# Kernel tuning notes

Measured on AMD Instinct MI355X. Metric: run time of the kernel, lower is better.

Reference implementation:

```python
import jax, jax.numpy as jnp
import numpy as np
import math

B, NRES, RPR = 1, 384, 3
L = NRES * RPR          # 1152 rigids
CS, CZ = 256, 128
CH, H, PQ, PV = 16, 8, 8, 12


def _ln(x, scale, bias):
    mu = jnp.mean(x, axis=-1, keepdims=True)
    var = jnp.var(x, axis=-1, keepdims=True)
    return (x - mu) * jax.lax.rsqrt(var + 1e-5) * scale + bias


def _quat_to_rot(q):
    q = q / jnp.linalg.norm(q, axis=-1, keepdims=True)
    w, x, y, z = q[..., 0], q[..., 1], q[..., 2], q[..., 3]
    r = jnp.stack([
        1 - 2 * (y * y + z * z), 2 * (x * y - w * z), 2 * (x * z + w * y),
        2 * (x * y + w * z), 1 - 2 * (x * x + z * z), 2 * (y * z - w * x),
        2 * (x * z - w * y), 2 * (y * z + w * x), 1 - 2 * (x * x + y * y),
    ], axis=-1)
    return r.reshape(q.shape[:-1] + (3, 3))


def setup_inputs() -> dict:
    key = jax.random.key(0)
    ks = jax.random.split(key, 20)
    s = jax.random.normal(ks[0], (B, L, CS), jnp.float32)
    z = jax.random.normal(ks[1], (B, NRES, NRES, CZ), jnp.float32)
    rot = _quat_to_rot(jax.random.normal(ks[2], (B, L, 4), jnp.float32))
    trans = 10.0 * jax.random.normal(ks[3], (B, L, 3), jnp.float32)
    mask = jnp.ones((B, L), jnp.float32)
    rigid_to_res_idx = jnp.broadcast_to(jnp.arange(L, dtype=jnp.int32) // RPR, (B, L))
    w = lambda k, sh: 0.02 * jax.random.normal(k, sh, jnp.float32)
    return {
        "s": s, "z": z, "rot": rot, "trans": trans, "mask": mask,
        "ln_s_scale": jnp.ones((CS,), jnp.float32), "ln_s_bias": jnp.zeros((CS,), jnp.float32),
        "ln_z_scale": jnp.ones((CZ,), jnp.float32), "ln_z_bias": jnp.zeros((CZ,), jnp.float32),
        "w_q": w(ks[4], (CS, H * CH)), "w_k": w(ks[5], (CS, H * CH)), "w_v": w(ks[6], (CS, H * CH)),
        "w_qp": w(ks[7], (CS, H * PQ * 3)), "w_kp": w(ks[8], (CS, H * PQ * 3)), "w_vp": w(ks[9], (CS, H * PV * 3)),
        "w_b": w(ks[10], (CZ, H)),
        "head_weights": jnp.full((H,), 0.5413, jnp.float32),  # softplus^-1(1)
        "w_out": w(ks[11], (H * (CH + CZ + PV * 4), CS)),
        "b_out": jnp.zeros((CS,), jnp.float32),
        "rigid_to_res_idx": rigid_to_res_idx,
    }


def reference(s, z, rot, trans, mask, ln_s_scale, ln_s_bias, ln_z_scale, ln_z_bias,
              w_q, w_k, w_v, w_qp, w_kp, w_vp, w_b, head_weights, w_out, b_out,
              rigid_to_res_idx):
    b_, l_ = s.shape[0], s.shape[1]
    idx = rigid_to_res_idx[0]                       # [L] rigid -> residue, shared over batch
    s_ln = _ln(s, ln_s_scale, ln_s_bias)            # [B,L,CS]
    z_ln = _ln(z, ln_z_scale, ln_z_bias)            # [B,N,N,CZ]

    q = (s_ln @ w_q).reshape(b_, l_, H, CH)
    k = (s_ln @ w_k).reshape(b_, l_, H, CH)
    v = (s_ln @ w_v).reshape(b_, l_, H, CH)

    # local points, then rigid-transform to global frame: x_g = R x + t
    q_p = (s_ln @ w_qp).reshape(b_, l_, H, PQ, 3)
    k_p = (s_ln @ w_kp).reshape(b_, l_, H, PQ, 3)
    v_p = (s_ln @ w_vp).reshape(b_, l_, H, PV, 3)
    t5 = trans[:, :, None, None, :]
    q_g = jnp.einsum("blij,blhpj->blhpi", rot, q_p) + t5
    k_g = jnp.einsum("blij,blhpj->blhpi", rot, k_p) + t5
    v_g = jnp.einsum("blij,blhpj->blhpi", rot, v_p) + t5

    # scalar qk term
    a = jnp.einsum("blhc,bjhc->bhlj", q, k) * math.sqrt(1.0 / (3 * CH))
    # pair bias, broadcast residue-pair -> rigid-pair
    b_res = z_ln @ w_b                                # [B,N,N,H]
    b_full = b_res[:, idx][:, :, idx]                 # [B,L,L,H]
    a = a + math.sqrt(1.0 / 3) * jnp.transpose(b_full, (0, 3, 1, 2))
    # point-distance term: ||q-k||^2 = |q|^2 + |k|^2 - 2 q.k (summed over P,3)
    hw = jax.nn.softplus(head_weights) * math.sqrt(1.0 / (3 * (PQ * 9.0 / 2)))
    qq = jnp.sum(q_g * q_g, axis=(-1, -2)).transpose(0, 2, 1)   # [B,H,L]
    kk = jnp.sum(k_g * k_g, axis=(-1, -2)).transpose(0, 2, 1)
    qk = jnp.einsum("blhpc,bjhpc->bhlj", q_g, k_g)
    d2 = qq[:, :, :, None] + kk[:, :, None, :] - 2.0 * qk
    a = a - 0.5 * d2 * hw[None, :, None, None]
    a = a + (mask[:, None, None, :] - 1.0) * 1e9
    attn = jax.nn.softmax(a, axis=-1)                 # [B,H,L,L]

    o = jnp.einsum("bhlj,bjhc->blhc", attn, v)        # [B,L,H,CH]
    o_pt_g = jnp.einsum("bhlj,bjhpc->blhpc", attn, v_g)
    # back to local frame of query rigid: R^T (x - t)
    o_pt = jnp.einsum("blji,blhpj->blhpi", rot, o_pt_g - t5)
    o_pt_norm = jnp.sqrt(jnp.sum(o_pt * o_pt, axis=-1) + 1e-8)  # [B,L,H,PV]
    # pair output: sum attention over rigids belonging to each key residue
    attn_res = attn.reshape(b_, H, l_, NRES, RPR).sum(-1)       # [B,H,L,N]
    z_l = z_ln[:, idx]                                           # [B,L,N,CZ]
    o_pair = jnp.einsum("bhln,blnc->blhc", attn_res, z_l)        # [B,L,H,CZ]

    cat = jnp.concatenate(
        [o, o_pt.reshape(b_, l_, H, PV * 3), o_pt_norm, o_pair], axis=-1
    ).reshape(b_, l_, H * (CH + PV * 4 + CZ))
    return cat @ w_out + b_out                        # [B,L,CS]
```

## Files before the change

kernel.cpp:

```cpp
#include <hip/hip_runtime.h>
#include <hip/hip_bf16.h>

#define L 1152
#define NRES 384
#define CS 256
#define CZ 128
#define H 8
#define CH 16
#define PQ 8
#define PV 12
#define PSTR 1088

#define OFF_SLN  0L
#define OFF_PROJ 294912L
#define OFF_WPK  1548288L
#define OFF_QCAT 1826816L
#define OFF_KCAT 2232320L
#define OFF_VCAT 2637824L
#define OFF_BRES 3227648L
#define OFF_MURS 4407296L
#define OFF_ATTN 4702208L
#define OFF_CAT  15319040L
#define OFF_PAV  18286592L
#define OFF_POP  21825536L
#define OFF_ARES 26544128L
#define OFF_PCAT 30083072L
#define OFF_RST  32442368L

__global__ __launch_bounds__(256) void k_pre(
    const float* wq, const float* wk, const float* wv,
    const float* wqp, const float* wkp, const float* wvp, float* wpack,
    const float* s, const float* lnss, const float* lnsb, float* sln,
    const float* z, const float* lnzs, const float* lnzb,
    const float* wb, float* murs, float* bres_t){
  int bx = blockIdx.x, t = threadIdx.x;
  if(bx < 256){
    int k = bx;
    for(int c=t; c<PSTR; c+=256){
      float v;
      if(c<128)        v = wq [(long)k*128 + c];
      else if(c<256)   v = wk [(long)k*128 + c-128];
      else if(c<384)   v = wv [(long)k*128 + c-256];
      else if(c<576)   v = wqp[(long)k*192 + c-384];
      else if(c<768)   v = wkp[(long)k*192 + c-576];
      else if(c<1056)  v = wvp[(long)k*288 + c-768];
      else             v = 0.f;
      wpack[(long)k*PSTR + c] = v;
    }
    return;
  }
  if(bx < 256 + L){
    int l = bx - 256;
    __shared__ float red[CS];
    float x = s[(long)l*CS + t];
    red[t] = x; __syncthreads();
    for(int st=128; st>0; st>>=1){ if(t<st) red[t]+=red[t+st]; __syncthreads(); }
    float mu = red[0] * (1.f/CS); __syncthreads();
    float d = x - mu;
    red[t] = d*d; __syncthreads();
    for(int st=128; st>0; st>>=1){ if(t<st) red[t]+=red[t+st]; __syncthreads(); }
    float var = red[0]*(1.f/CS);
    sln[(long)l*CS + t] = d*rsqrtf(var + 1e-5f)*lnss[t] + lnsb[t];
    return;
  }
  {
    long rp0 = (long)(bx - 256 - L)*32;
    int r = t>>3, part = t&7;
    long rp = rp0 + r;
    __shared__ __align__(16) float swb[8*132];
    __shared__ float SB[8][2];
    const float4* z4 = (const float4*)z;
    float4 x0 = z4[rp*32 + part*4 + 0];
    float4 x1 = z4[rp*32 + part*4 + 1];
    float4 x2 = z4[rp*32 + part*4 + 2];
    float4 x3 = z4[rp*32 + part*4 + 3];
    #pragma unroll
    for(int k2=0;k2<4;k2++){
      int e = t + k2*256; int h = e>>7, c = e&127;
      swb[h*132 + c] = lnzs[c]*wb[(long)c*8 + h];
    }
    __syncthreads();
    if(t < 64){
      int h = t>>3, seg = t&7;
      float S=0, Bv=0;
      #pragma unroll
      for(int i=0;i<16;i++){
        int c = seg*16+i;
        S  += swb[h*132+c];
        Bv += lnzb[c]*wb[(long)c*8 + h];
      }
      #pragma unroll
      for(int off=1;off<8;off<<=1){ S += __shfl_xor(S,off,64); Bv += __shfl_xor(Bv,off,64); }
      if(seg==0){ SB[h][0]=S; SB[h][1]=Bv; }
    }
    float s1 = x0.x+x0.y+x0.z+x0.w + x1.x+x1.y+x1.z+x1.w
             + x2.x+x2.y+x2.z+x2.w + x3.x+x3.y+x3.z+x3.w;
    float s2 = x0.x*x0.x+x0.y*x0.y+x0.z*x0.z+x0.w*x0.w
             + x1.x*x1.x+x1.y*x1.y+x1.z*x1.z+x1.w*x1.w
             + x2.x*x2.x+x2.y*x2.y+x2.z*x2.z+x2.w*x2.w
             + x3.x*x3.x+x3.y*x3.y+x3.z*x3.z+x3.w*x3.w;
    #pragma unroll
    for(int off=1;off<8;off<<=1){ s1 += __shfl_xor(s1,off,64); s2 += __shfl_xor(s2,off,64); }
    float mu = s1*(1.f/CZ);
    float var = s2*(1.f/CZ) - mu*mu;
    float rstd = rsqrtf(var + 1e-5f);
    if(part==0){ murs[rp*2]=mu; murs[rp*2+1]=rstd; }
    float acc[8];
    const float4* swb4 = (const float4*)swb;
    #pragma unroll
    for(int h=0;h<8;h++){
      float4 wa = swb4[h*33 + part*4 + 0];
      float4 wbv= swb4[h*33 + part*4 + 1];
      float4 wc = swb4[h*33 + part*4 + 2];
      float4 wd = swb4[h*33 + part*4 + 3];
      acc[h] = x0.x*wa.x + x0.y*wa.y + x0.z*wa.z + x0.w*wa.w
             + x1.x*wbv.x+ x1.y*wbv.y+ x1.z*wbv.z+ x1.w*wbv.w
             + x2.x*wc.x + x2.y*wc.y + x2.z*wc.z + x2.w*wc.w
             + x3.x*wd.x + x3.y*wd.y + x3.z*wd.z + x3.w*wd.w;
    }
    #pragma unroll
    for(int off=1;off<8;off<<=1){
      #pragma unroll
      for(int h=0;h<8;h++) acc[h] += __shfl_xor(acc[h],off,64);
    }
    __syncthreads();
    if(part==0){
      #pragma unroll
      for(int h=0;h<8;h++)
        bres_t[(long)h*147456 + rp] = rstd*(acc[h] - mu*SB[h][0]) + SB[h][1];
    }
  }
}

__global__ __launch_bounds__(256) void k_proj(const float* sln, const float* wpack, float* proj){
  int l0 = blockIdx.x*64, c0 = blockIdx.y*64, t = threadIdx.x;
  __shared__ float a_s[32][68];
  __shared__ __align__(16) float w_s[32][68];
  int tr = t>>4, tc = t&15;
  float4 acc[4] = {{0,0,0,0},{0,0,0,0},{0,0,0,0},{0,0,0,0}};
  for(int kc=0; kc<8; kc++){
    int k0 = kc*32;
    {
      int row = t>>2, kk0 = (t&3)*8;
      const float4* src = (const float4*)(sln + (long)(l0+row)*256 + k0 + kk0);
      float4 v0 = src[0], v1 = src[1];
      a_s[kk0+0][row]=v0.x; a_s[kk0+1][row]=v0.y; a_s[kk0+2][row]=v0.z; a_s[kk0+3][row]=v0.w;
      a_s[kk0+4][row]=v1.x; a_s[kk0+5][row]=v1.y; a_s[kk0+6][row]=v1.z; a_s[kk0+7][row]=v1.w;
    }
    #pragma unroll
    for(int kk2=0; kk2<2; kk2++){
      int kk = (t>>4) + 16*kk2;
      *(float4*)&w_s[kk][(t&15)*4] = *(const float4*)(wpack + (long)(k0+kk)*PSTR + c0 + (t&15)*4);
    }
    __syncthreads();
    #pragma unroll 8
    for(int kk=0; kk<32; kk++){
      float4 a4 = *(const float4*)&a_s[kk][tr*4];
      float4 b4 = *(const float4*)&w_s[kk][tc*4];
      acc[0].x+=a4.x*b4.x; acc[0].y+=a4.x*b4.y; acc[0].z+=a4.x*b4.z; acc[0].w+=a4.x*b4.w;
      acc[1].x+=a4.y*b4.x; acc[1].y+=a4.y*b4.y; acc[1].z+=a4.y*b4.z; acc[1].w+=a4.y*b4.w;
      acc[2].x+=a4.z*b4.x; acc[2].y+=a4.z*b4.y; acc[2].z+=a4.z*b4.z; acc[2].w+=a4.z*b4.w;
      acc[3].x+=a4.w*b4.x; acc[3].y+=a4.w*b4.y; acc[3].z+=a4.w*b4.z; acc[3].w+=a4.w*b4.w;
    }
    __syncthreads();
  }
  #pragma unroll
  for(int r=0;r<4;r++)
    *(float4*)(proj + (long)(l0 + tr*4 + r)*PSTR + c0 + tc*4) = acc[r];
}

__global__ __launch_bounds__(256) void k_rigid(const float* proj, const float* rot, const float* trans,
                        const float* mask, const float* hws,
                        float* qcat, float* kcat, float* vcat){
  int l = blockIdx.x, t = threadIdx.x;
  __shared__ float R[9], T[3], hwS[8], qgs[192], kgs[192];
  if(t<9) R[t]=rot[(long)l*9+t];
  if(t<3) T[t]=trans[(long)l*3+t];
  if(t>=16 && t<24) hwS[t-16] = log1pf(expf(hws[t-16]))*0.09622504486493764f;
  __syncthreads();
  const float* pr = proj + (long)l*PSTR;
  if(t<128){
    int h=t>>4, c=t&15;
    qcat[((long)h*44 + c)*L + l] = 0.14433756729740643f * pr[t];
    kcat[((long)h*44 + c)*L + l] = pr[128+t];
    vcat[((long)h*L + l)*64 + c] = pr[256+t];
  }
  if(t < 192){
    int h=t/24, m=t%24, p=m/3, i=m%3;
    float qa = R[i*3+0]*pr[384+h*24+p*3+0] + R[i*3+1]*pr[384+h*24+p*3+1]
             + R[i*3+2]*pr[384+h*24+p*3+2] + T[i];
    float ka = R[i*3+0]*pr[576+h*24+p*3+0] + R[i*3+1]*pr[576+h*24+p*3+1]
             + R[i*3+2]*pr[576+h*24+p*3+2] + T[i];
    qgs[t]=qa; kgs[t]=ka;
    qcat[((long)h*44 + 16 + m)*L + l] = hwS[h]*qa;
    kcat[((long)h*44 + 16 + m)*L + l] = ka;
  }
  for(int it=t; it<288; it+=256){
    int h=it/36, m=it%36, p=m/3, i=m%3;
    float a = R[i*3+0]*pr[768+h*36+p*3+0] + R[i*3+1]*pr[768+h*36+p*3+1]
            + R[i*3+2]*pr[768+h*36+p*3+2] + T[i];
    vcat[((long)h*L + l)*64 + 16 + m] = a;
  }
  if(t < 96){
    int h=t/12, d=t%12;
    vcat[((long)h*L + l)*64 + 52 + d] = 0.f;
  }
  __syncthreads();
  if(t < 8){
    float qq=0, kk=0;
    #pragma unroll
    for(int m=0;m<24;m++){ qq += qgs[t*24+m]*qgs[t*24+m]; kk += kgs[t*24+m]*kgs[t*24+m]; }
    qcat[((long)t*44 + 40)*L + l] = -0.5f*hwS[t]*qq;
    kcat[((long)t*44 + 40)*L + l] = -0.5f*hwS[t]*kk + (mask[l]-1.f)*1e9f;
  }
}

__global__ __launch_bounds__(256) void k_scores(const float* qcat, const float* kcat,
                         const float* bres_t, float* attn){
  int l0 = blockIdx.x*32, j0 = blockIdx.y*128, h = blockIdx.z;
  int t = threadIdx.x;
  __shared__ __align__(16) float q_t[44*36];
  __shared__ __align__(16) float k_t[44*132];
  __shared__ float bp[12*44];
  int rl0 = l0/3, rj0 = j0/3;
  {
    const float* srcq = qcat + (long)h*44*L + l0;
    for(int i=t; i<44*32; i+=256){
      int c = i>>5, ll = i&31;
      q_t[c*36 + ll] = srcq[(long)c*L + ll];
    }
    const float* srck = kcat + (long)h*44*L + j0;
    for(int i=t; i<44*128; i+=256){
      int c = i>>7, jj = i&127;
      k_t[c*132 + jj] = srck[(long)c*L + jj];
    }
    const float* bb = bres_t + (long)h*147456;
    for(int i=t; i<12*44; i+=256){
      int r = i/44, c = i-r*44;
      int rr = rl0+r, cc = rj0+c;
      bp[i] = (rr<NRES && cc<NRES) ? bb[(long)rr*NRES + cc] : 0.f;
    }
  }
  __syncthreads();
  int lg = t>>5, jg = t&31;
  float acc[4][4] = {};
  #pragma unroll 4
  for(int c=0;c<40;c++){
    float4 qv = *(const float4*)&q_t[c*36 + lg*4];
    float4 kv = *(const float4*)&k_t[c*132 + jg*4];
    acc[0][0]+=qv.x*kv.x; acc[0][1]+=qv.x*kv.y; acc[0][2]+=qv.x*kv.z; acc[0][3]+=qv.x*kv.w;
    acc[1][0]+=qv.y*kv.x; acc[1][1]+=qv.y*kv.y; acc[1][2]+=qv.y*kv.z; acc[1][3]+=qv.y*kv.w;
    acc[2][0]+=qv.z*kv.x; acc[2][1]+=qv.z*kv.y; acc[2][2]+=qv.z*kv.z; acc[2][3]+=qv.z*kv.w;
    acc[3][0]+=qv.w*kv.x; acc[3][1]+=qv.w*kv.y; acc[3][2]+=qv.w*kv.z; acc[3][3]+=qv.w*kv.w;
  }
  float4 colc = *(const float4*)&k_t[40*132 + jg*4];
  int jb = j0 + jg*4;
  int rj0i = (jb  )/3 - rj0;
  int rj1i = (jb+1)/3 - rj0;
  int rj2i = (jb+2)/3 - rj0;
  int rj3i = (jb+3)/3 - rj0;
  #pragma unroll
  for(int r=0;r<4;r++){
    int row = lg*4+r;
    float rowc = q_t[40*36 + row];
    const float* bpr = &bp[((l0+row)/3 - rl0)*44];
    float4 o;
    o.x = __expf(acc[r][0] + rowc + colc.x + 0.5773502691896258f*bpr[rj0i]);
    o.y = __expf(acc[r][1] + rowc + colc.y + 0.5773502691896258f*bpr[rj1i]);
    o.z = __expf(acc[r][2] + rowc + colc.z + 0.5773502691896258f*bpr[rj2i]);
    o.w = __expf(acc[r][3] + rowc + colc.w + 0.5773502691896258f*bpr[rj3i]);
    *(float4*)(attn + ((long)h*L + l0+row)*L + jb) = o;
  }
}

__global__ __launch_bounds__(256) void k_rowstat(const float* attn, float* rstat, float* ares){
  long row = (long)blockIdx.x*4 + (threadIdx.x>>6);
  int lane = threadIdx.x & 63;
  int w = threadIdx.x >> 6;
  __shared__ float es[4][1152];
  const float* p = attn + row*L;
  float v[18];
  float s=0;
  #pragma unroll
  for(int i=0;i<18;i++){ v[i]=p[lane + i*64]; s+=v[i]; }
  #pragma unroll
  for(int off=1;off<64;off<<=1) s+=__shfl_xor(s,off,64);
  float inv = 1.f/s;
  if(lane==0) rstat[row] = inv;
  #pragma unroll
  for(int i=0;i<18;i++) es[w][lane + i*64] = v[i]*inv;
  __syncthreads();
  #pragma unroll
  for(int q=0;q<6;q++){
    int n = lane + q*64;
    ares[row*NRES + n] = es[w][3*n] + es[w][3*n+1] + es[w][3*n+2];
  }
}

__global__ __launch_bounds__(256) void k_av(const float* attn, const float* vcat,
                     const float* rstat, float* pav){
  int lb = blockIdx.x, h = blockIdx.y, sp = blockIdx.z, t = threadIdx.x;
  int l0 = lb*64;
  __shared__ __align__(16) float a_s[64][68];
  __shared__ __align__(16) float v_s[64][68];
  int lgrp = t>>4, dgrp = t&15;
  float4 acc[4] = {{0,0,0,0},{0,0,0,0},{0,0,0,0},{0,0,0,0}};
  const float* abase = attn + ((long)h*L + l0)*L;
  int al = t>>2, jj0s = (t&3)*16;
  float irow = rstat[(long)h*L + l0 + al];
  for(int jc=sp*3; jc<sp*3+3; jc++){
    int j0 = jc*64;
    {
      const float4* src = (const float4*)(abase + (long)al*L + j0 + jj0s);
      float4 p0 = src[0], p1 = src[1], p2 = src[2], p3 = src[3];
      a_s[jj0s+ 0][al]=p0.x*irow; a_s[jj0s+ 1][al]=p0.y*irow;
      a_s[jj0s+ 2][al]=p0.z*irow; a_s[jj0s+ 3][al]=p0.w*irow;
      a_s[jj0s+ 4][al]=p1.x*irow; a_s[jj0s+ 5][al]=p1.y*irow;
      a_s[jj0s+ 6][al]=p1.z*irow; a_s[jj0s+ 7][al]=p1.w*irow;
      a_s[jj0s+ 8][al]=p2.x*irow; a_s[jj0s+ 9][al]=p2.y*irow;
      a_s[jj0s+10][al]=p2.z*irow; a_s[jj0s+11][al]=p2.w*irow;
      a_s[jj0s+12][al]=p3.x*irow; a_s[jj0s+13][al]=p3.y*irow;
      a_s[jj0s+14][al]=p3.z*irow; a_s[jj0s+15][al]=p3.w*irow;
    }
    {
      int jj = t>>2, seg = t&3;
      const float4* src = (const float4*)(vcat + ((long)h*L + j0 + jj)*64 + seg*16);
      float4 q0=src[0], q1=src[1], q2=src[2], q3=src[3];
      float4* dst = (float4*)&v_s[jj][seg*16];
      dst[0]=q0; dst[1]=q1; dst[2]=q2; dst[3]=q3;
    }
    __syncthreads();
    #pragma unroll 8
    for(int jj=0; jj<64; jj++){
      float4 av = *(const float4*)&a_s[jj][lgrp*4];
      float4 vv = *(const float4*)&v_s[jj][dgrp*4];
      acc[0].x+=av.x*vv.x; acc[0].y+=av.x*vv.y; acc[0].z+=av.x*vv.z; acc[0].w+=av.x*vv.w;
      acc[1].x+=av.y*vv.x; acc[1].y+=av.y*vv.y; acc[1].z+=av.y*vv.z; acc[1].w+=av.y*vv.w;
      acc[2].x+=av.z*vv.x; acc[2].y+=av.z*vv.y; acc[2].z+=av.z*vv.z; acc[2].w+=av.z*vv.w;
      acc[3].x+=av.w*vv.x; acc[3].y+=av.w*vv.y; acc[3].z+=av.w*vv.z; acc[3].w+=av.w*vv.w;
    }
    __syncthreads();
  }
  #pragma unroll
  for(int r=0;r<4;r++)
    *(float4*)(pav + (((long)sp*H + h)*L + l0 + lgrp*4 + r)*64 + dgrp*4) = acc[r];
}

#define OPAIR_STEP(Z0,Z1,Z2,Z3,NB) { \
    float4 a0 = *(const float4*)&ar[0][th][NB]; \
    float4 a1 = *(const float4*)&ar[1][th][NB]; \
    float4 a2 = *(const float4*)&ar[2][th][NB]; \
    acc[0][0] += a0.x*Z0.x + a0.y*Z1.x + a0.z*Z2.x + a0.w*Z3.x; \
    acc[0][1] += a0.x*Z0.y + a0.y*Z1.y + a0.z*Z2.y + a0.w*Z3.y; \
    acc[0][2] += a0.x*Z0.z + a0.y*Z1.z + a0.z*Z2.z + a0.w*Z3.z; \
    acc[0][3] += a0.x*Z0.w + a0.y*Z1.w + a0.z*Z2.w + a0.w*Z3.w; \
    acc[1][0] += a1.x*Z0.x + a1.y*Z1.x + a1.z*Z2.x + a1.w*Z3.x; \
    acc[1][1] += a1.x*Z0.y + a1.y*Z1.y + a1.z*Z2.y + a1.w*Z3.y; \
    acc[1][2] += a1.x*Z0.z + a1.y*Z1.z + a1.z*Z2.z + a1.w*Z3.z; \
    acc[1][3] += a1.x*Z0.w + a1.y*Z1.w + a1.z*Z2.w + a1.w*Z3.w; \
    acc[2][0] += a2.x*Z0.x + a2.y*Z1.x + a2.z*Z2.x + a2.w*Z3.x; \
    acc[2][1] += a2.x*Z0.y + a2.y*Z1.y + a2.z*Z2.y + a2.w*Z3.y; \
    acc[2][2] += a2.x*Z0.z + a2.y*Z1.z + a2.z*Z2.z + a2.w*Z3.z; \
    acc[2][3] += a2.x*Z0.w + a2.y*Z1.w + a2.z*Z2.w + a2.w*Z3.w; }

__global__ __launch_bounds__(256) void k_opair(const float* ares, const float* z, const float* murs,
                        const float* sc, const int* ridx, float* po){
  int r=blockIdx.x, sp=blockIdx.y, t=threadIdx.x;
  __shared__ __align__(16) float ar[3][H][96];
  __shared__ __align__(16) float mrs[96*2];
  __shared__ float S1s[24];
  int rl = ridx[r*3];
  int n0 = sp*96;
  int tc = t&31, th = t>>5;
  const float* zbase = z + ((long)(rl*NRES + n0))*CZ + tc*4;
  float4 zc0 = *(const float4*)(zbase + 0L*CZ);
  float4 zc1 = *(const float4*)(zbase + 1L*CZ);
  float4 zc2 = *(const float4*)(zbase + 2L*CZ);
  float4 zc3 = *(const float4*)(zbase + 3L*CZ);
  for(int i=t;i<192;i+=256) mrs[i]=murs[((long)rl*NRES + n0)*2 + i];
  __syncthreads();
  for(int it=t; it<3*H*96; it+=256){
    int lo = it/(H*96);
    int rem = it - lo*(H*96);
    int h = rem/96, n = rem - h*96;
    ar[lo][h][n] = ares[((long)h*L + r*3+lo)*NRES + n0 + n] * mrs[n*2+1];
  }
  __syncthreads();
  if(t<192){
    int row=t>>3, seg=t&7;
    const float* arr = ((const float*)ar) + row*96 + seg*12;
    const float* mur = mrs + seg*24;
    float s1=0;
    #pragma unroll
    for(int q2=0;q2<12;q2++) s1 += arr[q2]*mur[q2*2];
    s1 += __shfl_xor(s1,1,64); s1 += __shfl_xor(s1,2,64); s1 += __shfl_xor(s1,4,64);
    if(seg==0) S1s[row]=s1;
  }
  __syncthreads();
  float acc[3][4]={};
  for(int nb=0; nb<88; nb+=8){
    float4 zn0 = *(const float4*)(zbase + (long)(nb+4)*CZ);
    float4 zn1 = *(const float4*)(zbase + (long)(nb+5)*CZ);
    float4 zn2 = *(const float4*)(zbase + (long)(nb+6)*CZ);
    float4 zn3 = *(const float4*)(zbase + (long)(nb+7)*CZ);
    OPAIR_STEP(zc0,zc1,zc2,zc3, nb);
    zc0 = *(const float4*)(zbase + (long)(nb+ 8)*CZ);
    zc1 = *(const float4*)(zbase + (long)(nb+ 9)*CZ);
    zc2 = *(const float4*)(zbase + (long)(nb+10)*CZ);
    zc3 = *(const float4*)(zbase + (long)(nb+11)*CZ);
    OPAIR_STEP(zn0,zn1,zn2,zn3, nb+4);
  }
  {
    float4 zn0 = *(const float4*)(zbase + 92L*CZ);
    float4 zn1 = *(const float4*)(zbase + 93L*CZ);
    float4 zn2 = *(const float4*)(zbase + 94L*CZ);
    float4 zn3 = *(const float4*)(zbase + 95L*CZ);
    OPAIR_STEP(zc0,zc1,zc2,zc3, 88);
    OPAIR_STEP(zn0,zn1,zn2,zn3, 92);
  }
  float4 sc4 = *(const float4*)(sc + tc*4);
  #pragma unroll
  for(int lo=0;lo<3;lo++){
    float s1v = S1s[lo*8+th];
    float4 o = { sc4.x*(acc[lo][0]-s1v), sc4.y*(acc[lo][1]-s1v),
                 sc4.z*(acc[lo][2]-s1v), sc4.w*(acc[lo][3]-s1v) };
    *(float4*)(po + ((long)sp*L + (long)(r*3+lo))*1024 + th*128 + tc*4) = o;
  }
}

__global__ __launch_bounds__(256) void k_post(const float* pav, const float* rot, const float* trans,
                        const float* po, const float* bi, float* cat){
  int bx = blockIdx.x, t = threadIdx.x;
  if(bx < 288){
    int lb = bx % 36, h = bx / 36;
    int l0 = lb*32;
    __shared__ __align__(16) float fin_s[32][64];
    #pragma unroll
    for(int k=0;k<2;k++){
      int fi = t + k*256;
      int l = fi>>4, c4 = fi&15;
      long base = (((long)h)*L + l0 + l)*64 + c4*4;
      float4 r = {0,0,0,0};
      #pragma unroll
      for(int p=0;p<6;p++){
        float4 a = *(const float4*)(pav + (long)p*589824 + base);
        r.x+=a.x; r.y+=a.y; r.z+=a.z; r.w+=a.w;
      }
      *(float4*)&fin_s[l][c4*4] = r;
    }
    __syncthreads();
    for(int it=t; it<32*16; it+=256){
      int l=it>>4, c=it&15;
      cat[(long)(l0+l)*1536 + h*192 + c] = fin_s[l][c];
    }
    for(int it=t; it<32*12; it+=256){
      int l=it/12, p=it%12;
      long gl = l0+l;
      float og0 = fin_s[l][16+p*3+0]-trans[gl*3+0];
      float og1 = fin_s[l][16+p*3+1]-trans[gl*3+1];
      float og2 = fin_s[l][16+p*3+2]-trans[gl*3+2];
      float* crow = cat + gl*1536 + h*192;
      float nrm=0;
      #pragma unroll
      for(int i=0;i<3;i++){
        float v = rot[gl*9+0+i]*og0 + rot[gl*9+3+i]*og1 + rot[gl*9+6+i]*og2;
        crow[16+p*3+i]=v; nrm+=v*v;
      }
      crow[52+p]=sqrtf(nrm+1e-8f);
    }
    return;
  }
  {
    int i = (bx-288)*256 + t;
    const float4* p = (const float4*)po;
    float4 a = p[i], b = p[i + 294912], c = p[i + 589824], d = p[i + 884736];
    int l = i>>8, rem = i&255;
    int h = rem>>5, c4 = rem&31;
    float4 bv = ((const float4*)bi)[c4];
    float4 r = {a.x+b.x+c.x+d.x+bv.x, a.y+b.y+c.y+d.y+bv.y,
                a.z+b.z+c.z+d.z+bv.z, a.w+b.w+c.w+d.w+bv.w};
    ((float4*)cat)[(long)l*384 + h*48 + 16 + c4] = r;
  }
}

__global__ __launch_bounds__(256) void k_final(const float* cat, const float* wout, float* pcat){
  int l0 = blockIdx.x*64, c0 = blockIdx.y*64, kp = blockIdx.z, t = threadIdx.x;
  __shared__ __align__(16) float a_s[64][68];
  __shared__ __align__(16) float w_s[64][68];
  int lgrp = t>>4, cgrp = t&15;
  float4 acc[4] = {{0,0,0,0},{0,0,0,0},{0,0,0,0},{0,0,0,0}};
  int al = t>>2, ks0 = (t&3)*16;
  for(int kc=0; kc<3; kc++){
    int k0 = kp*192 + kc*64;
    {
      const float4* src = (const float4*)(cat + (long)(l0+al)*1536 + k0 + ks0);
      float4 p0 = src[0], p1 = src[1], p2 = src[2], p3 = src[3];
      a_s[ks0+ 0][al]=p0.x; a_s[ks0+ 1][al]=p0.y; a_s[ks0+ 2][al]=p0.z; a_s[ks0+ 3][al]=p0.w;
      a_s[ks0+ 4][al]=p1.x; a_s[ks0+ 5][al]=p1.y; a_s[ks0+ 6][al]=p1.z; a_s[ks0+ 7][al]=p1.w;
      a_s[ks0+ 8][al]=p2.x; a_s[ks0+ 9][al]=p2.y; a_s[ks0+10][al]=p2.z; a_s[ks0+11][al]=p2.w;
      a_s[ks0+12][al]=p3.x; a_s[ks0+13][al]=p3.y; a_s[ks0+14][al]=p3.z; a_s[ks0+15][al]=p3.w;
    }
    {
      int kk = t>>2, seg = t&3;
      const float4* src = (const float4*)(wout + (long)(k0+kk)*256 + c0 + seg*16);
      float4 q0=src[0], q1=src[1], q2=src[2], q3=src[3];
      float4* dst = (float4*)&w_s[kk][seg*16];
      dst[0]=q0; dst[1]=q1; dst[2]=q2; dst[3]=q3;
    }
    __syncthreads();
    #pragma unroll 8
    for(int kk=0; kk<64; kk++){
      float4 av = *(const float4*)&a_s[kk][lgrp*4];
      float4 wv = *(const float4*)&w_s[kk][cgrp*4];
      acc[0].x+=av.x*wv.x; acc[0].y+=av.x*wv.y; acc[0].z+=av.x*wv.z; acc[0].w+=av.x*wv.w;
      acc[1].x+=av.y*wv.x; acc[1].y+=av.y*wv.y; acc[1].z+=av.y*wv.z; acc[1].w+=av.y*wv.w;
      acc[2].x+=av.z*wv.x; acc[2].y+=av.z*wv.y; acc[2].z+=av.z*wv.z; acc[2].w+=av.z*wv.w;
      acc[3].x+=av.w*wv.x; acc[3].y+=av.w*wv.y; acc[3].z+=av.w*wv.z; acc[3].w+=av.w*wv.w;
    }
    __syncthreads();
  }
  #pragma unroll
  for(int r=0;r<4;r++)
    *(float4*)(pcat + ((long)kp*L + l0 + lgrp*4 + r)*256 + c0 + cgrp*4) = acc[r];
}

__global__ __launch_bounds__(256) void k_redout(const float* pcat, const float* bout, float* out){
  int i = blockIdx.x*256 + threadIdx.x;
  const float4* p = (const float4*)pcat;
  float4 bv = ((const float4*)bout)[i&63];
  float4 r = bv;
  #pragma unroll
  for(int p8=0;p8<8;p8++){
    float4 a = p[i + (long)p8*73728];
    r.x+=a.x; r.y+=a.y; r.z+=a.z; r.w+=a.w;
  }
  ((float4*)out)[i] = r;
}

extern "C" void kernel_launch(void* const* d_in, const int* in_sizes, int n_in,
                              void* d_out, int out_size, void* d_ws, size_t ws_size,
                              hipStream_t stream) {
  const float* s      = (const float*)d_in[0];
  const float* z      = (const float*)d_in[1];
  const float* rot    = (const float*)d_in[2];
  const float* trans  = (const float*)d_in[3];
  const float* mask   = (const float*)d_in[4];
  const float* lnss   = (const float*)d_in[5];
  const float* lnsb   = (const float*)d_in[6];
  const float* lnzs   = (const float*)d_in[7];
  const float* lnzb   = (const float*)d_in[8];
  const float* wq     = (const float*)d_in[9];
  const float* wk     = (const float*)d_in[10];
  const float* wv     = (const float*)d_in[11];
  const float* wqp    = (const float*)d_in[12];
  const float* wkp    = (const float*)d_in[13];
  const float* wvp    = (const float*)d_in[14];
  const float* wb     = (const float*)d_in[15];
  const float* hws    = (const float*)d_in[16];
  const float* wout   = (const float*)d_in[17];
  const float* bout   = (const float*)d_in[18];
  const int*  ridx    = (const int*)d_in[19];

  float* ws  = (float*)d_ws;
  float* out = (float*)d_out;

  float* sln  = ws + OFF_SLN;
  float* proj = ws + OFF_PROJ;
  float* wpk  = ws + OFF_WPK;
  float* qcat = ws + OFF_QCAT;
  float* kcat = ws + OFF_KCAT;
  float* vcat = ws + OFF_VCAT;
  float* bres = ws + OFF_BRES;
  float* murs = ws + OFF_MURS;
  float* attn = ws + OFF_ATTN;
  float* cat  = ws + OFF_CAT;
  float* pcat = ws + OFF_PCAT;
  float* pav  = ws + OFF_PAV;
  float* po   = ws + OFF_POP;
  float* ares = ws + OFF_ARES;
  float* rst  = ws + OFF_RST;

  k_pre<<<dim3(256 + L + NRES*NRES/32), dim3(256), 0, stream>>>(
      wq, wk, wv, wqp, wkp, wvp, wpk,
      s, lnss, lnsb, sln,
      z, lnzs, lnzb, wb, murs, bres);
  k_proj<<<dim3(18,17), dim3(256), 0, stream>>>(sln, wpk, proj);
  k_rigid<<<dim3(L), dim3(256), 0, stream>>>(proj, rot, trans, mask, hws, qcat, kcat, vcat);
  k_scores<<<dim3(L/32, L/128, H), dim3(256), 0, stream>>>(qcat, kcat, bres, attn);
  k_rowstat<<<dim3(H*L/4), dim3(256), 0, stream>>>(attn, rst, ares);
  k_av<<<dim3(L/64, H, 6), dim3(256), 0, stream>>>(attn, vcat, rst, pav);
  k_opair<<<dim3(NRES, 4), dim3(256), 0, stream>>>(ares, z, murs, lnzs, ridx, po);
  k_post<<<dim3(288 + 1152), dim3(256), 0, stream>>>(pav, rot, trans, po, lnzb, cat);
  k_final<<<dim3(L/64, 4, 8), dim3(256), 0, stream>>>(cat, wout, pcat);
  k_redout<<<dim3(288), dim3(256), 0, stream>>>(pcat, bout, out);
}
```

Baseline: 298.2 us.

## Merge rowstat with AV and opair with post-AV via block-index dispatch

Row-sum normalization is deferred out of the AV loop. The AV blocks now read raw exp scores and run in the same launch as the row-stat blocks, with the 1/sum scale applied later when the partial AV sums are reduced. The opair computation and the AV post-processing are merged into one launch, and the pair-output reduction is split into its own small kernel. The aim is to remove launch gaps and serialization between independent stages, at the cost of shared-memory aliasing and heterogeneous blocks inside each launch.

```diff
diff --git a/kernel.cpp b/kernel.cpp
--- a/kernel.cpp
+++ b/kernel.cpp
@@ -273,54 +273,54 @@
   }
 }
 
-__global__ __launch_bounds__(256) void k_rowstat(const float* attn, float* rstat, float* ares){
-  long row = (long)blockIdx.x*4 + (threadIdx.x>>6);
-  int lane = threadIdx.x & 63;
-  int w = threadIdx.x >> 6;
-  __shared__ float es[4][1152];
-  const float* p = attn + row*L;
-  float v[18];
-  float s=0;
-  #pragma unroll
-  for(int i=0;i<18;i++){ v[i]=p[lane + i*64]; s+=v[i]; }
-  #pragma unroll
-  for(int off=1;off<64;off<<=1) s+=__shfl_xor(s,off,64);
-  float inv = 1.f/s;
-  if(lane==0) rstat[row] = inv;
-  #pragma unroll
-  for(int i=0;i<18;i++) es[w][lane + i*64] = v[i]*inv;
-  __syncthreads();
-  #pragma unroll
-  for(int q=0;q<6;q++){
-    int n = lane + q*64;
-    ares[row*NRES + n] = es[w][3*n] + es[w][3*n+1] + es[w][3*n+2];
-  }
-}
-
-__global__ __launch_bounds__(256) void k_av(const float* attn, const float* vcat,
-                     const float* rstat, float* pav){
-  int lb = blockIdx.x, h = blockIdx.y, sp = blockIdx.z, t = threadIdx.x;
+__global__ __launch_bounds__(256) void k_rsav(const float* attn, const float* vcat,
+                     float* rstat, float* ares, float* pav){
+  __shared__ __align__(16) float smem[2*64*68];
+  int bx = blockIdx.x, t = threadIdx.x;
+  if(bx < 2304){
+    float (*es)[1152] = (float(*)[1152])smem;
+    long row = (long)bx*4 + (t>>6);
+    int lane = t & 63;
+    int w = t >> 6;
+    const float* p = attn + row*L;
+    float v[18];
+    float s=0;
+    #pragma unroll
+    for(int i=0;i<18;i++){ v[i]=p[lane + i*64]; s+=v[i]; }
+    #pragma unroll
+    for(int off=1;off<64;off<<=1) s+=__shfl_xor(s,off,64);
+    float inv = 1.f/s;
+    if(lane==0) rstat[row] = inv;
+    #pragma unroll
+    for(int i=0;i<18;i++) es[w][lane + i*64] = v[i]*inv;
+    __syncthreads();
+    #pragma unroll
+    for(int q=0;q<6;q++){
+      int n = lane + q*64;
+      ares[row*NRES + n] = es[w][3*n] + es[w][3*n+1] + es[w][3*n+2];
+    }
+    return;
+  }
+  int bx2 = bx - 2304;
+  int lb = bx2 % 18;
+  int rest = bx2 / 18;
+  int h = rest & 7, sp = rest >> 3;
   int l0 = lb*64;
-  __shared__ __align__(16) float a_s[64][68];
-  __shared__ __align__(16) float v_s[64][68];
+  float (*a_s)[68] = (float(*)[68])smem;
+  float (*v_s)[68] = (float(*)[68])(smem + 64*68);
   int lgrp = t>>4, dgrp = t&15;
   float4 acc[4] = {{0,0,0,0},{0,0,0,0},{0,0,0,0},{0,0,0,0}};
   const float* abase = attn + ((long)h*L + l0)*L;
   int al = t>>2, jj0s = (t&3)*16;
-  float irow = rstat[(long)h*L + l0 + al];
   for(int jc=sp*3; jc<sp*3+3; jc++){
     int j0 = jc*64;
     {
       const float4* src = (const float4*)(abase + (long)al*L + j0 + jj0s);
       float4 p0 = src[0], p1 = src[1], p2 = src[2], p3 = src[3];
-      a_s[jj0s+ 0][al]=p0.x*irow; a_s[jj0s+ 1][al]=p0.y*irow;
-      a_s[jj0s+ 2][al]=p0.z*irow; a_s[jj0s+ 3][al]=p0.w*irow;
-      a_s[jj0s+ 4][al]=p1.x*irow; a_s[jj0s+ 5][al]=p1.y*irow;
-      a_s[jj0s+ 6][al]=p1.z*irow; a_s[jj0s+ 7][al]=p1.w*irow;
-      a_s[jj0s+ 8][al]=p2.x*irow; a_s[jj0s+ 9][al]=p2.y*irow;
-      a_s[jj0s+10][al]=p2.z*irow; a_s[jj0s+11][al]=p2.w*irow;
-      a_s[jj0s+12][al]=p3.x*irow; a_s[jj0s+13][al]=p3.y*irow;
-      a_s[jj0s+14][al]=p3.z*irow; a_s[jj0s+15][al]=p3.w*irow;
+      a_s[jj0s+ 0][al]=p0.x; a_s[jj0s+ 1][al]=p0.y; a_s[jj0s+ 2][al]=p0.z; a_s[jj0s+ 3][al]=p0.w;
+      a_s[jj0s+ 4][al]=p1.x; a_s[jj0s+ 5][al]=p1.y; a_s[jj0s+ 6][al]=p1.z; a_s[jj0s+ 7][al]=p1.w;
+      a_s[jj0s+ 8][al]=p2.x; a_s[jj0s+ 9][al]=p2.y; a_s[jj0s+10][al]=p2.z; a_s[jj0s+11][al]=p2.w;
+      a_s[jj0s+12][al]=p3.x; a_s[jj0s+13][al]=p3.y; a_s[jj0s+14][al]=p3.z; a_s[jj0s+15][al]=p3.w;
     }
     {
       int jj = t>>2, seg = t&3;
@@ -363,78 +363,81 @@
     acc[2][2] += a2.x*Z0.z + a2.y*Z1.z + a2.z*Z2.z + a2.w*Z3.z; \
     acc[2][3] += a2.x*Z0.w + a2.y*Z1.w + a2.z*Z2.w + a2.w*Z3.w; }
 
-__global__ __launch_bounds__(256) void k_opair(const float* ares, const float* z, const float* murs,
-                        const float* sc, const int* ridx, float* po){
-  int r=blockIdx.x, sp=blockIdx.y, t=threadIdx.x;
-  __shared__ __align__(16) float ar[3][H][96];
-  __shared__ __align__(16) float mrs[96*2];
-  __shared__ float S1s[24];
-  int rl = ridx[r*3];
-  int n0 = sp*96;
-  int tc = t&31, th = t>>5;
-  const float* zbase = z + ((long)(rl*NRES + n0))*CZ + tc*4;
-  float4 zc0 = *(const float4*)(zbase + 0L*CZ);
-  float4 zc1 = *(const float4*)(zbase + 1L*CZ);
-  float4 zc2 = *(const float4*)(zbase + 2L*CZ);
-  float4 zc3 = *(const float4*)(zbase + 3L*CZ);
-  for(int i=t;i<192;i+=256) mrs[i]=murs[((long)rl*NRES + n0)*2 + i];
-  __syncthreads();
-  for(int it=t; it<3*H*96; it+=256){
-    int lo = it/(H*96);
-    int rem = it - lo*(H*96);
-    int h = rem/96, n = rem - h*96;
-    ar[lo][h][n] = ares[((long)h*L + r*3+lo)*NRES + n0 + n] * mrs[n*2+1];
-  }
-  __syncthreads();
-  if(t<192){
-    int row=t>>3, seg=t&7;
-    const float* arr = ((const float*)ar) + row*96 + seg*12;
-    const float* mur = mrs + seg*24;
-    float s1=0;
-    #pragma unroll
-    for(int q2=0;q2<12;q2++) s1 += arr[q2]*mur[q2*2];
-    s1 += __shfl_xor(s1,1,64); s1 += __shfl_xor(s1,2,64); s1 += __shfl_xor(s1,4,64);
-    if(seg==0) S1s[row]=s1;
-  }
-  __syncthreads();
-  float acc[3][4]={};
-  for(int nb=0; nb<88; nb+=8){
-    float4 zn0 = *(const float4*)(zbase + (long)(nb+4)*CZ);
-    float4 zn1 = *(const float4*)(zbase + (long)(nb+5)*CZ);
-    float4 zn2 = *(const float4*)(zbase + (long)(nb+6)*CZ);
-    float4 zn3 = *(const float4*)(zbase + (long)(nb+7)*CZ);
-    OPAIR_STEP(zc0,zc1,zc2,zc3, nb);
-    zc0 = *(const float4*)(zbase + (long)(nb+ 8)*CZ);
-    zc1 = *(const float4*)(zbase + (long)(nb+ 9)*CZ);
-    zc2 = *(const float4*)(zbase + (long)(nb+10)*CZ);
-    zc3 = *(const float4*)(zbase + (long)(nb+11)*CZ);
-    OPAIR_STEP(zn0,zn1,zn2,zn3, nb+4);
+__global__ __launch_bounds__(256) void k_oppA(const float* ares, const float* z, const float* murs,
+                        const float* sc, const int* ridx, float* po,
+                        const float* pav, const float* rstat,
+                        const float* rot, const float* trans, float* cat){
+  __shared__ __align__(16) float smem[2560];
+  int bx = blockIdx.x, t = threadIdx.x;
+  if(bx < 1536){
+    int r = bx >> 2, sp = bx & 3;
+    float (*ar)[H][96] = (float(*)[H][96])smem;
+    float* mrs = smem + 2304;
+    float* S1s = smem + 2496;
+    int rl = ridx[r*3];
+    int n0 = sp*96;
+    int tc = t&31, th = t>>5;
+    const float* zbase = z + ((long)(rl*NRES + n0))*CZ + tc*4;
+    float4 zc0 = *(const float4*)(zbase + 0L*CZ);
+    float4 zc1 = *(const float4*)(zbase + 1L*CZ);
+    float4 zc2 = *(const float4*)(zbase + 2L*CZ);
+    float4 zc3 = *(const float4*)(zbase + 3L*CZ);
+    for(int i=t;i<192;i+=256) mrs[i]=murs[((long)rl*NRES + n0)*2 + i];
+    __syncthreads();
+    for(int it=t; it<3*H*96; it+=256){
+      int lo = it/(H*96);
+      int rem = it - lo*(H*96);
+      int h = rem/96, n = rem - h*96;
+      ar[lo][h][n] = ares[((long)h*L + r*3+lo)*NRES + n0 + n] * mrs[n*2+1];
+    }
+    __syncthreads();
+    if(t<192){
+      int row=t>>3, seg=t&7;
+      const float* arr = ((const float*)ar) + row*96 + seg*12;
+      const float* mur = mrs + seg*24;
+      float s1=0;
+      #pragma unroll
+      for(int q2=0;q2<12;q2++) s1 += arr[q2]*mur[q2*2];
+      s1 += __shfl_xor(s1,1,64); s1 += __shfl_xor(s1,2,64); s1 += __shfl_xor(s1,4,64);
+      if(seg==0) S1s[row]=s1;
+    }
+    __syncthreads();
+    float acc[3][4]={};
+    for(int nb=0; nb<88; nb+=8){
+      float4 zn0 = *(const float4*)(zbase + (long)(nb+4)*CZ);
+      float4 zn1 = *(const float4*)(zbase + (long)(nb+5)*CZ);
+      float4 zn2 = *(const float4*)(zbase + (long)(nb+6)*CZ);
+      float4 zn3 = *(const float4*)(zbase + (long)(nb+7)*CZ);
+      OPAIR_STEP(zc0,zc1,zc2,zc3, nb);
+      zc0 = *(const float4*)(zbase + (long)(nb+ 8)*CZ);
+      zc1 = *(const float4*)(zbase + (long)(nb+ 9)*CZ);
+      zc2 = *(const float4*)(zbase + (long)(nb+10)*CZ);
+      zc3 = *(const float4*)(zbase + (long)(nb+11)*CZ);
+      OPAIR_STEP(zn0,zn1,zn2,zn3, nb+4);
+    }
+    {
+      float4 zn0 = *(const float4*)(zbase + 92L*CZ);
+      float4 zn1 = *(const float4*)(zbase + 93L*CZ);
+      float4 zn2 = *(const float4*)(zbase + 94L*CZ);
+      float4 zn3 = *(const float4*)(zbase + 95L*CZ);
+      OPAIR_STEP(zc0,zc1,zc2,zc3, 88);
+      OPAIR_STEP(zn0,zn1,zn2,zn3, 92);
+    }
+    float4 sc4 = *(const float4*)(sc + tc*4);
+    #pragma unroll
+    for(int lo=0;lo<3;lo++){
+      float s1v = S1s[lo*8+th];
+      float4 o = { sc4.x*(acc[lo][0]-s1v), sc4.y*(acc[lo][1]-s1v),
+                   sc4.z*(acc[lo][2]-s1v), sc4.w*(acc[lo][3]-s1v) };
+      *(float4*)(po + ((long)sp*L + (long)(r*3+lo))*1024 + th*128 + tc*4) = o;
+    }
+    return;
   }
   {
-    float4 zn0 = *(const float4*)(zbase + 92L*CZ);
-    float4 zn1 = *(const float4*)(zbase + 93L*CZ);
-    float4 zn2 = *(const float4*)(zbase + 94L*CZ);
-    float4 zn3 = *(const float4*)(zbase + 95L*CZ);
-    OPAIR_STEP(zc0,zc1,zc2,zc3, 88);
-    OPAIR_STEP(zn0,zn1,zn2,zn3, 92);
-  }
-  float4 sc4 = *(const float4*)(sc + tc*4);
-  #pragma unroll
-  for(int lo=0;lo<3;lo++){
-    float s1v = S1s[lo*8+th];
-    float4 o = { sc4.x*(acc[lo][0]-s1v), sc4.y*(acc[lo][1]-s1v),
-                 sc4.z*(acc[lo][2]-s1v), sc4.w*(acc[lo][3]-s1v) };
-    *(float4*)(po + ((long)sp*L + (long)(r*3+lo))*1024 + th*128 + tc*4) = o;
-  }
-}
-
-__global__ __launch_bounds__(256) void k_post(const float* pav, const float* rot, const float* trans,
-                        const float* po, const float* bi, float* cat){
-  int bx = blockIdx.x, t = threadIdx.x;
-  if(bx < 288){
-    int lb = bx % 36, h = bx / 36;
+    int bx2 = bx - 1536;
+    int lb = bx2 % 36, h = bx2 / 36;
     int l0 = lb*32;
-    __shared__ __align__(16) float fin_s[32][64];
+    float (*fin_s)[64] = (float(*)[64])smem;
     #pragma unroll
     for(int k=0;k<2;k++){
       int fi = t + k*256;
@@ -446,6 +449,8 @@
         float4 a = *(const float4*)(pav + (long)p*589824 + base);
         r.x+=a.x; r.y+=a.y; r.z+=a.z; r.w+=a.w;
       }
+      float inv = rstat[(long)h*L + l0 + l];
+      r.x*=inv; r.y*=inv; r.z*=inv; r.w*=inv;
       *(float4*)&fin_s[l][c4*4] = r;
     }
     __syncthreads();
@@ -468,19 +473,19 @@
       }
       crow[52+p]=sqrtf(nrm+1e-8f);
     }
-    return;
-  }
-  {
-    int i = (bx-288)*256 + t;
-    const float4* p = (const float4*)po;
-    float4 a = p[i], b = p[i + 294912], c = p[i + 589824], d = p[i + 884736];
-    int l = i>>8, rem = i&255;
-    int h = rem>>5, c4 = rem&31;
-    float4 bv = ((const float4*)bi)[c4];
-    float4 r = {a.x+b.x+c.x+d.x+bv.x, a.y+b.y+c.y+d.y+bv.y,
-                a.z+b.z+c.z+d.z+bv.z, a.w+b.w+c.w+d.w+bv.w};
-    ((float4*)cat)[(long)l*384 + h*48 + 16 + c4] = r;
-  }
+  }
+}
+
+__global__ __launch_bounds__(256) void k_postB(const float* po, const float* bi, float* cat){
+  int i = blockIdx.x*256 + threadIdx.x;
+  const float4* p = (const float4*)po;
+  float4 a = p[i], b = p[i + 294912], c = p[i + 589824], d = p[i + 884736];
+  int l = i>>8, rem = i&255;
+  int h = rem>>5, c4 = rem&31;
+  float4 bv = ((const float4*)bi)[c4];
+  float4 r = {a.x+b.x+c.x+d.x+bv.x, a.y+b.y+c.y+d.y+bv.y,
+              a.z+b.z+c.z+d.z+bv.z, a.w+b.w+c.w+d.w+bv.w};
+  ((float4*)cat)[(long)l*384 + h*48 + 16 + c4] = r;
 }
 
 __global__ __launch_bounds__(256) void k_final(const float* cat, const float* wout, float* pcat){
@@ -587,10 +592,10 @@
   k_proj<<<dim3(18,17), dim3(256), 0, stream>>>(sln, wpk, proj);
   k_rigid<<<dim3(L), dim3(256), 0, stream>>>(proj, rot, trans, mask, hws, qcat, kcat, vcat);
   k_scores<<<dim3(L/32, L/128, H), dim3(256), 0, stream>>>(qcat, kcat, bres, attn);
-  k_rowstat<<<dim3(H*L/4), dim3(256), 0, stream>>>(attn, rst, ares);
-  k_av<<<dim3(L/64, H, 6), dim3(256), 0, stream>>>(attn, vcat, rst, pav);
-  k_opair<<<dim3(NRES, 4), dim3(256), 0, stream>>>(ares, z, murs, lnzs, ridx, po);
-  k_post<<<dim3(288 + 1152), dim3(256), 0, stream>>>(pav, rot, trans, po, lnzb, cat);
+  k_rsav<<<dim3(2304 + 864), dim3(256), 0, stream>>>(attn, vcat, rst, ares, pav);
+  k_oppA<<<dim3(1536 + 288), dim3(256), 0, stream>>>(ares, z, murs, lnzs, ridx, po,
+                                                     pav, rst, rot, trans, cat);
+  k_postB<<<dim3(1152), dim3(256), 0, stream>>>(po, lnzb, cat);
   k_final<<<dim3(L/64, 4, 8), dim3(256), 0, stream>>>(cat, wout, pcat);
   k_redout<<<dim3(288), dim3(256), 0, stream>>>(pcat, bout, out);
 }
```

Measured after the change: 295.3 us, median of 2. No clear change (-1.0%).
